# Optimization experiments

Hardware: AMD Instinct MI355X
Metric: run time of the kernel (lower is better)

The kernel has to match this reference:

```python
import jax, jax.numpy as jnp
import numpy as np

T, B, D, E, H = 64, 1024, 128, 256, 512


def _gru(x_emb, h0, W_ih, W_hh, b_ih, b_hh):
    """Standard GRU (PyTorch gate convention) over time-major x_emb [T,B,E]."""
    xW = x_emb @ W_ih + b_ih  # [T,B,3H], precompute input contractions

    def step(h, xw):
        hW = h @ W_hh + b_hh
        xr, xz, xn = jnp.split(xw, 3, axis=-1)
        hr, hz, hn = jnp.split(hW, 3, axis=-1)
        r = jax.nn.sigmoid(xr + hr)
        z = jax.nn.sigmoid(xz + hz)
        n = jnp.tanh(xn + r * hn)
        h_new = (1.0 - z) * n + z * h
        return h_new, h_new

    h_t, ys = jax.lax.scan(step, h0, xW)
    return ys, h_t


def setup_inputs() -> dict:
    key = jax.random.key(0)
    ks = jax.random.split(key, 16)
    s_in = 1.0 / np.sqrt(D)
    s_emb = 1.0 / np.sqrt(E)
    s_hid = 1.0 / np.sqrt(H)
    return {
        "past_input": jax.random.normal(ks[0], (T, B, D), jnp.float32),
        "future_input": jax.random.normal(ks[1], (T, B, D), jnp.float32),
        "noise": jax.random.normal(ks[2], (B, H), jnp.float32),
        "W_emb": jax.random.normal(ks[3], (D, E), jnp.float32) * s_in,
        "b_emb": jnp.zeros((E,), jnp.float32),
        "W_ih_enc": jax.random.normal(ks[4], (E, 3 * H), jnp.float32) * s_emb,
        "W_hh_enc": jax.random.normal(ks[5], (H, 3 * H), jnp.float32) * s_hid,
        "b_ih_enc": jnp.zeros((3 * H,), jnp.float32),
        "b_hh_enc": jnp.zeros((3 * H,), jnp.float32),
        "W_ih_dec": jax.random.normal(ks[6], (E, 3 * H), jnp.float32) * s_emb,
        "W_hh_dec": jax.random.normal(ks[7], (H, 3 * H), jnp.float32) * s_hid,
        "b_ih_dec": jnp.zeros((3 * H,), jnp.float32),
        "b_hh_dec": jnp.zeros((3 * H,), jnp.float32),
        "W_out": jax.random.normal(ks[8], (H, D), jnp.float32) * s_hid,
        "b_out": jnp.zeros((D,), jnp.float32),
    }


def reference(past_input, future_input, noise, W_emb, b_emb,
              W_ih_enc, W_hh_enc, b_ih_enc, b_hh_enc,
              W_ih_dec, W_hh_dec, b_ih_dec, b_hh_dec,
              W_out, b_out):
    past_emb = jax.nn.relu(past_input @ W_emb + b_emb)      # [T,B,E]
    fut_emb = jax.nn.relu(future_input @ W_emb + b_emb)     # [T,B,E]

    h0 = jnp.zeros((past_emb.shape[1], W_hh_enc.shape[0]), past_emb.dtype)
    _, h_t = _gru(past_emb, h0, W_ih_enc, W_hh_enc, b_ih_enc, b_hh_enc)

    # shift future embedding: step 0 -> zeros, step t -> emb at t-1
    fut_shift = jnp.concatenate([jnp.zeros_like(fut_emb[:1]), fut_emb[:-1]], axis=0)

    hidden = h_t + noise
    future_target, _ = _gru(fut_shift, hidden, W_ih_dec, W_hh_dec, b_ih_dec, b_hh_dec)
    return future_target @ W_out + b_out  # [T,B,D]
```

## Files before the change

kernel.cpp:

```cpp
#include <hip/hip_runtime.h>

typedef __bf16 bf16;
typedef __bf16 bf16x8 __attribute__((ext_vector_type(8)));
typedef float f32x4 __attribute__((ext_vector_type(4)));

#define Tt 64
#define Bb 1024
#define Dd 128
#define Ee 256
#define Hh 512
#define H3 1536

__device__ __forceinline__ float sigmf(float x) { return 1.0f / (1.0f + __expf(-x)); }
__device__ __forceinline__ float tanhfast(float x) {
    float e = __expf(2.0f * x);
    return 1.0f - 2.0f / (e + 1.0f);
}

#define LD_SC(dst, bp, OFF) \
    asm volatile("global_load_dwordx4 %0, %1, off offset:" #OFF " sc1" : "=v"(dst) : "v"(bp))
#define ST_SC(bp, OFF, val) \
    asm volatile("global_store_short %0, %1, off offset:" #OFF " sc1" :: "v"(bp), "v"(val))

__global__ void k_prep(const float* __restrict__ We, const float* __restrict__ Wie, const float* __restrict__ Whe,
                       const float* __restrict__ Wid, const float* __restrict__ Whd, const float* __restrict__ Wo,
                       bf16* __restrict__ dWe, bf16* __restrict__ dWie, bf16* __restrict__ dWhe,
                       bf16* __restrict__ dWid, bf16* __restrict__ dWhd, bf16* __restrict__ dWo) {
    long i = (long)blockIdx.x * 256 + threadIdx.x;
    const float* s;
    bf16* d;
    int K, N;
    if (i < 32768) { s = We; d = dWe; K = Dd; N = Ee; }
    else if ((i -= 32768) < 393216) { s = Wie; d = dWie; K = Ee; N = H3; }
    else if ((i -= 393216) < 786432) { s = Whe; d = dWhe; K = Hh; N = H3; }
    else if ((i -= 786432) < 393216) { s = Wid; d = dWid; K = Ee; N = H3; }
    else if ((i -= 393216) < 786432) { s = Whd; d = dWhd; K = Hh; N = H3; }
    else if ((i -= 786432) < 65536) { s = Wo; d = dWo; K = Hh; N = Dd; }
    else return;
    int n = (int)(i / K), k = (int)(i - (long)n * K);
    d[i] = (bf16)s[(size_t)k * N + n];
}

__global__ __launch_bounds__(256) void k_embed(const float* __restrict__ xP, const float* __restrict__ xF,
                                               const bf16* __restrict__ WT, const float* __restrict__ bias,
                                               bf16* __restrict__ oP, bf16* __restrict__ oF) {
    const int lane = threadIdx.x & 63, wv = threadIdx.x >> 6;
    const float* x = blockIdx.z ? xF : xP;
    bf16* o = blockIdx.z ? oF : oP;
    const int m0w = blockIdx.x * 128 + wv * 32;
    const int c0 = blockIdx.y * 64;
    const int koff = (lane >> 4) * 8;
    f32x4 acc[2][4];
#pragma unroll
    for (int m = 0; m < 2; ++m)
#pragma unroll
        for (int s = 0; s < 4; ++s) acc[m][s] = f32x4{0.f, 0.f, 0.f, 0.f};

    const float* xp0 = x + (size_t)(m0w + (lane & 15)) * Dd + koff;
#pragma unroll
    for (int kc = 0; kc < 4; ++kc) {
        bf16x8 a0, a1;
        {
            float4 f0 = *(const float4*)(xp0 + kc * 32);
            float4 f1 = *(const float4*)(xp0 + kc * 32 + 4);
            a0[0] = (bf16)f0.x; a0[1] = (bf16)f0.y; a0[2] = (bf16)f0.z; a0[3] = (bf16)f0.w;
            a0[4] = (bf16)f1.x; a0[5] = (bf16)f1.y; a0[6] = (bf16)f1.z; a0[7] = (bf16)f1.w;
            float4 g0 = *(const float4*)(xp0 + 16 * Dd + kc * 32);
            float4 g1 = *(const float4*)(xp0 + 16 * Dd + kc * 32 + 4);
            a1[0] = (bf16)g0.x; a1[1] = (bf16)g0.y; a1[2] = (bf16)g0.z; a1[3] = (bf16)g0.w;
            a1[4] = (bf16)g1.x; a1[5] = (bf16)g1.y; a1[6] = (bf16)g1.z; a1[7] = (bf16)g1.w;
        }
#pragma unroll
        for (int s = 0; s < 4; ++s) {
            bf16x8 b = *(const bf16x8*)(WT + (size_t)(c0 + s * 16 + (lane & 15)) * Dd + kc * 32 + koff);
            acc[0][s] = __builtin_amdgcn_mfma_f32_16x16x32_bf16(a0, b, acc[0][s], 0, 0, 0);
            acc[1][s] = __builtin_amdgcn_mfma_f32_16x16x32_bf16(a1, b, acc[1][s], 0, 0, 0);
        }
    }
#pragma unroll
    for (int m = 0; m < 2; ++m)
#pragma unroll
        for (int s = 0; s < 4; ++s) {
            int col = c0 + s * 16 + (lane & 15);
            float bv = bias[col];
#pragma unroll
            for (int r = 0; r < 4; ++r) {
                int row = m0w + m * 16 + (lane >> 4) * 4 + r;
                o[(size_t)row * Ee + col] = (bf16)fmaxf(acc[m][s][r] + bv, 0.0f);
            }
        }
}

__global__ __launch_bounds__(512, 1) void k_gru_all(
    const bf16* __restrict__ embP, const bf16* __restrict__ embF, const float* __restrict__ noise,
    const bf16* __restrict__ WihE, const bf16* __restrict__ WhhE,
    const float* __restrict__ bIhE, const float* __restrict__ bHhE,
    const bf16* __restrict__ WihD, const bf16* __restrict__ WhhD,
    const float* __restrict__ bIhD, const float* __restrict__ bHhD,
    bf16* __restrict__ hA, bf16* __restrict__ hB, bf16* __restrict__ ys, unsigned* __restrict__ flags) {
    __shared__ bf16 Wih[6 * 8 * 64 * 8];
    __shared__ bf16 Whh[6 * 16 * 64 * 8];
    const int tid = threadIdx.x;
    const int lane = tid & 63, wv = tid >> 6;
    const int bid = blockIdx.x;
    const int im = (bid & 7) * 2 + (bid >> 7);
    const int in = (bid >> 3) & 15;
    const int rh = wv >> 1, ch = wv & 1;
    const int rowb = im * 64 + rh * 16;
    const int arow0 = rowb + (lane & 15);
    const int koff = (lane >> 4) * 8;
    const int colc = in * 32 + ch * 16 + (lane & 15);
    unsigned* dom = flags + ((size_t)im * 4 + rh) * 32;
    const int myidx = in * 2 + ch;

    const bf16x8* WihV = (const bf16x8*)Wih;
    const bf16x8* WhhV = (const bf16x8*)Whh;

    auto stage = [&](const bf16* WT, int Kdim, int KC, bf16* lds) {
        int total = 6 * KC * 64;
        for (int idx = tid; idx < total; idx += 512) {
            int ln = idx & 63;
            int kc = (idx >> 6) % KC;
            int s = (idx >> 6) / KC;
            int gate = s >> 1, f = s & 1;
            int col = gate * Hh + in * 32 + f * 16 + (ln & 15);
            int k = kc * 32 + (ln >> 4) * 8;
            *(bf16x8*)(lds + (size_t)idx * 8) = *(const bf16x8*)(WT + (size_t)col * Kdim + k);
        }
    };

    float bi[3], bh[3];
    auto load_bias = [&](const float* bIh, const float* bHh) {
#pragma unroll
        for (int g = 0; g < 3; ++g) {
            bi[g] = bIh[g * Hh + colc];
            bh[g] = bHh[g * Hh + colc];
        }
    };

    auto signal = [&](unsigned seq) {
        asm volatile("s_waitcnt vmcnt(0)" ::: "memory");
        if (lane == 0) {
            unsigned* fp = dom + myidx;
            asm volatile("global_store_dword %0, %1, off sc1" :: "v"(fp), "v"(seq) : "memory");
        }
    };
    auto poll = [&](unsigned seq) -> unsigned long long {
        unsigned v;
        const unsigned* fp = dom + (lane & 31);
        asm volatile("global_load_dword %0, %1, off sc1\n\ts_waitcnt vmcnt(0)"
                     : "=v"(v) : "v"(fp) : "memory");
        return __ballot((int)(v >= seq));
    };
    auto wait_all = [&](unsigned seq) {
        while (poll(seq) != ~0ULL) __builtin_amdgcn_s_sleep(2);
    };

    f32x4 aR, aZ, aNX, aNH;
    auto zacc = [&]() {
        aR = f32x4{0.f, 0.f, 0.f, 0.f};
        aZ = f32x4{0.f, 0.f, 0.f, 0.f};
        aNX = f32x4{0.f, 0.f, 0.f, 0.f};
        aNH = f32x4{0.f, 0.f, 0.f, 0.f};
    };

    auto xp_phase = [&](const bf16* xp) {
        const bf16* ap = xp + (size_t)arow0 * Ee + koff;
#pragma unroll
        for (int kc = 0; kc < 8; ++kc) {
            bf16x8 a = *(const bf16x8*)(ap + kc * 32);
            aR = __builtin_amdgcn_mfma_f32_16x16x32_bf16(a, WihV[((0 + ch) * 8 + kc) * 64 + lane], aR, 0, 0, 0);
            aZ = __builtin_amdgcn_mfma_f32_16x16x32_bf16(a, WihV[((2 + ch) * 8 + kc) * 64 + lane], aZ, 0, 0, 0);
            aNX = __builtin_amdgcn_mfma_f32_16x16x32_bf16(a, WihV[((4 + ch) * 8 + kc) * 64 + lane], aNX, 0, 0, 0);
        }
    };

    auto hw_phase = [&](const bf16* hp, unsigned seq) {
        const bf16* h0p = hp + (size_t)arow0 * Hh + koff;
        bf16x8 h0[16];
        unsigned long long rdy = poll(seq);
#define HSTEP(p, OFF) \
        while (((rdy >> (2 * p)) & 3ULL) != 3ULL) { __builtin_amdgcn_s_sleep(2); rdy = poll(seq); } \
        LD_SC(h0[p], h0p, OFF);
        HSTEP(0, 0)    HSTEP(1, 64)   HSTEP(2, 128)  HSTEP(3, 192)
        HSTEP(4, 256)  HSTEP(5, 320)  HSTEP(6, 384)  HSTEP(7, 448)
        HSTEP(8, 512)  HSTEP(9, 576)  HSTEP(10, 640) HSTEP(11, 704)
        HSTEP(12, 768) HSTEP(13, 832) HSTEP(14, 896) HSTEP(15, 960)
#undef HSTEP
        asm volatile("s_waitcnt vmcnt(0)" ::: "memory");
        __builtin_amdgcn_sched_barrier(0);
#pragma unroll
        for (int kc = 0; kc < 16; ++kc) {
            aR = __builtin_amdgcn_mfma_f32_16x16x32_bf16(h0[kc], WhhV[((0 + ch) * 16 + kc) * 64 + lane], aR, 0, 0, 0);
            aZ = __builtin_amdgcn_mfma_f32_16x16x32_bf16(h0[kc], WhhV[((2 + ch) * 16 + kc) * 64 + lane], aZ, 0, 0, 0);
            aNH = __builtin_amdgcn_mfma_f32_16x16x32_bf16(h0[kc], WhhV[((4 + ch) * 16 + kc) * 64 + lane], aNH, 0, 0, 0);
        }
    };

    float hreg[4];
#pragma unroll
    for (int i = 0; i < 4; ++i) hreg[i] = 0.0f;

    auto epi = [&](bf16* op) {
        bf16* stb = op + (size_t)(rowb + (lane >> 4) * 4) * Hh + colc;
        unsigned short us[4];
#pragma unroll
        for (int r = 0; r < 4; ++r) {
            float rg = sigmf(aR[r] + bi[0] + bh[0]);
            float zg = sigmf(aZ[r] + bi[1] + bh[1]);
            float ng = tanhfast(aNX[r] + bi[2] + rg * (aNH[r] + bh[2]));
            float hv = (1.0f - zg) * ng + zg * hreg[r];
            hreg[r] = hv;
            us[r] = __builtin_bit_cast(unsigned short, (bf16)hv);
        }
        ST_SC(stb, 0, us[0]);
        ST_SC(stb, 1024, us[1]);
        ST_SC(stb, 2048, us[2]);
        ST_SC(stb, 3072, us[3]);
    };

    stage(WihE, Ee, 8, Wih);
    stage(WhhE, Hh, 16, Whh);
    load_bias(bIhE, bHhE);
    __syncthreads();

#pragma unroll 1
    for (int t = 0; t < Tt; ++t) {
        zacc();
        xp_phase(embP + (size_t)t * Bb * Ee);
        if (t > 0) hw_phase(((t - 1) & 1) ? hB : hA, (unsigned)t);
        epi((t & 1) ? hB : hA);
        signal((unsigned)(t + 1));
    }

    wait_all((unsigned)Tt);
    {
        bf16* stb = hA + (size_t)(rowb + (lane >> 4) * 4) * Hh + colc;
        unsigned short us[4];
#pragma unroll
        for (int r = 0; r < 4; ++r) {
            int row = rowb + (lane >> 4) * 4 + r;
            float v = hreg[r] + noise[(size_t)row * Hh + colc];
            hreg[r] = v;
            us[r] = __builtin_bit_cast(unsigned short, (bf16)v);
        }
        ST_SC(stb, 0, us[0]);
        ST_SC(stb, 1024, us[1]);
        ST_SC(stb, 2048, us[2]);
        ST_SC(stb, 3072, us[3]);
    }
    __syncthreads();
    stage(WihD, Ee, 8, Wih);
    stage(WhhD, Hh, 16, Whh);
    __syncthreads();
    load_bias(bIhD, bHhD);
    signal((unsigned)(Tt + 1));

#pragma unroll 1
    for (int t = 0; t < Tt; ++t) {
        zacc();
        if (t > 0) xp_phase(embF + (size_t)(t - 1) * Bb * Ee);
        hw_phase(t ? ys + (size_t)(t - 1) * Bb * Hh : hA, (unsigned)(Tt + 1 + t));
        epi(ys + (size_t)t * Bb * Hh);
        if (t < Tt - 1) signal((unsigned)(Tt + 2 + t));
    }
}

__global__ __launch_bounds__(256) void k_out(const bf16* __restrict__ ys, const bf16* __restrict__ WT,
                                             const float* __restrict__ bias, float* __restrict__ out) {
    const int lane = threadIdx.x & 63, wv = threadIdx.x >> 6;
    const int m0w = blockIdx.x * 256 + wv * 64;
    const int c0 = blockIdx.y * 64;
    const int koff = (lane >> 4) * 8;
    f32x4 acc[4][4];
#pragma unroll
    for (int m = 0; m < 4; ++m)
#pragma unroll
        for (int s = 0; s < 4; ++s) acc[m][s] = f32x4{0.f, 0.f, 0.f, 0.f};

    const bf16* ap = ys + (size_t)(m0w + (lane & 15)) * Hh + koff;
#pragma unroll
    for (int kc = 0; kc < 16; ++kc) {
        bf16x8 a0 = *(const bf16x8*)(ap + kc * 32);
        bf16x8 a1 = *(const bf16x8*)(ap + 16 * Hh + kc * 32);
        bf16x8 a2 = *(const bf16x8*)(ap + 32 * Hh + kc * 32);
        bf16x8 a3 = *(const bf16x8*)(ap + 48 * Hh + kc * 32);
#pragma unroll
        for (int s = 0; s < 4; ++s) {
            bf16x8 b = *(const bf16x8*)(WT + (size_t)(c0 + s * 16 + (lane & 15)) * Hh + kc * 32 + koff);
            acc[0][s] = __builtin_amdgcn_mfma_f32_16x16x32_bf16(a0, b, acc[0][s], 0, 0, 0);
            acc[1][s] = __builtin_amdgcn_mfma_f32_16x16x32_bf16(a1, b, acc[1][s], 0, 0, 0);
            acc[2][s] = __builtin_amdgcn_mfma_f32_16x16x32_bf16(a2, b, acc[2][s], 0, 0, 0);
            acc[3][s] = __builtin_amdgcn_mfma_f32_16x16x32_bf16(a3, b, acc[3][s], 0, 0, 0);
        }
    }
#pragma unroll
    for (int m = 0; m < 4; ++m)
#pragma unroll
        for (int s = 0; s < 4; ++s) {
            int col = c0 + s * 16 + (lane & 15);
            float bv = bias[col];
#pragma unroll
            for (int r = 0; r < 4; ++r) {
                int row = m0w + m * 16 + (lane >> 4) * 4 + r;
                out[(size_t)row * Dd + col] = acc[m][s][r] + bv;
            }
        }
}

extern "C" void kernel_launch(void* const* d_in, const int* in_sizes, int n_in,
                              void* d_out, int out_size, void* d_ws, size_t ws_size,
                              hipStream_t stream) {
    const float* past = (const float*)d_in[0];
    const float* fut = (const float*)d_in[1];
    const float* noise = (const float*)d_in[2];
    const float* W_emb = (const float*)d_in[3];
    const float* b_emb = (const float*)d_in[4];
    const float* W_ih_enc = (const float*)d_in[5];
    const float* W_hh_enc = (const float*)d_in[6];
    const float* b_ih_enc = (const float*)d_in[7];
    const float* b_hh_enc = (const float*)d_in[8];
    const float* W_ih_dec = (const float*)d_in[9];
    const float* W_hh_dec = (const float*)d_in[10];
    const float* b_ih_dec = (const float*)d_in[11];
    const float* b_hh_dec = (const float*)d_in[12];
    const float* W_out = (const float*)d_in[13];
    const float* b_out = (const float*)d_in[14];
    float* out = (float*)d_out;

    char* w = (char*)d_ws;
    auto alloc = [&](size_t bytes) {
        char* p = w;
        w += (bytes + 255) & ~(size_t)255;
        return p;
    };
    bf16* embP = (bf16*)alloc((size_t)Tt * Bb * Ee * 2);
    bf16* embF = (bf16*)alloc((size_t)Tt * Bb * Ee * 2);
    bf16* ys = (bf16*)alloc((size_t)Tt * Bb * Hh * 2);
    bf16* hA = (bf16*)alloc((size_t)Bb * Hh * 2);
    bf16* hB = (bf16*)alloc((size_t)Bb * Hh * 2);
    bf16* WembT = (bf16*)alloc((size_t)Ee * Dd * 2);
    bf16* WihEncT = (bf16*)alloc((size_t)H3 * Ee * 2);
    bf16* WhhEncT = (bf16*)alloc((size_t)H3 * Hh * 2);
    bf16* WihDecT = (bf16*)alloc((size_t)H3 * Ee * 2);
    bf16* WhhDecT = (bf16*)alloc((size_t)H3 * Hh * 2);
    bf16* WoutT = (bf16*)alloc((size_t)Dd * Hh * 2);
    unsigned* flags = (unsigned*)alloc(16 * 4 * 32 * sizeof(unsigned));

    k_prep<<<9600, 256, 0, stream>>>(W_emb, W_ih_enc, W_hh_enc, W_ih_dec, W_hh_dec, W_out,
                                     WembT, WihEncT, WhhEncT, WihDecT, WhhDecT, WoutT);

    k_embed<<<dim3(Tt * Bb / 128, Ee / 64, 2), 256, 0, stream>>>(past, fut, WembT, b_emb, embP, embF);

    hipMemsetAsync(flags, 0, 16 * 4 * 32 * sizeof(unsigned), stream);

    void* args[] = {(void*)&embP, (void*)&embF, (void*)&noise,
                    (void*)&WihEncT, (void*)&WhhEncT, (void*)&b_ih_enc, (void*)&b_hh_enc,
                    (void*)&WihDecT, (void*)&WhhDecT, (void*)&b_ih_dec, (void*)&b_hh_dec,
                    (void*)&hA, (void*)&hB, (void*)&ys, (void*)&flags};
    hipLaunchCooperativeKernel((const void*)k_gru_all, dim3(256), dim3(512), args, 0, stream);

    k_out<<<dim3(Tt * Bb / 256, Dd / 64), 256, 0, stream>>>(ys, WoutT, b_out, out);
}
```

Before: 1.040 ms.

## Restructure persistent GRU kernel: register-resident weights, LDS-staged hidden state, 32x32 MFMA

The recurrent kernel now keeps each wave's slice of the input and hidden weights in registers instead of LDS. Each block cooperatively stages its 32-row tile of the previous hidden state into swizzled LDS and runs 32x32x16 MFMAs. Gate pre-activations go through an LDS plane so four waves can run a vectorized epilogue that writes with dwordx4 stores. Synchronisation changes to one flag per block over 8 column-blocks instead of fine-grained per-wave polling. The aim is to cut LDS weight traffic and narrow store and poll overhead, at the cost of heavy register pressure (48 bf16x8 weight fragments per lane), extra block barriers and a coarser wait that can no longer overlap loads with partial readiness.

```diff
diff --git a/kernel.cpp b/kernel.cpp
--- a/kernel.cpp
+++ b/kernel.cpp
@@ -3,6 +3,7 @@
 typedef __bf16 bf16;
 typedef __bf16 bf16x8 __attribute__((ext_vector_type(8)));
 typedef float f32x4 __attribute__((ext_vector_type(4)));
+typedef float f32x16 __attribute__((ext_vector_type(16)));
 
 #define Tt 64
 #define Bb 1024
@@ -17,10 +18,10 @@
     return 1.0f - 2.0f / (e + 1.0f);
 }
 
-#define LD_SC(dst, bp, OFF) \
-    asm volatile("global_load_dwordx4 %0, %1, off offset:" #OFF " sc1" : "=v"(dst) : "v"(bp))
-#define ST_SC(bp, OFF, val) \
-    asm volatile("global_store_short %0, %1, off offset:" #OFF " sc1" :: "v"(bp), "v"(val))
+#define LD_SC(dst, bp) \
+    asm volatile("global_load_dwordx4 %0, %1, off sc1" : "=v"(dst) : "v"(bp))
+#define ST_SCX4(bp, val) \
+    asm volatile("global_store_dwordx4 %0, %1, off sc1" :: "v"(bp), "v"(val))
 
 __global__ void k_prep(const float* __restrict__ We, const float* __restrict__ Wie, const float* __restrict__ Whe,
                        const float* __restrict__ Wid, const float* __restrict__ Whd, const float* __restrict__ Wo,
@@ -91,177 +92,219 @@
         }
 }
 
-__global__ __launch_bounds__(512, 1) void k_gru_all(
+__global__ __launch_bounds__(384, 2) void k_gru_all(
     const bf16* __restrict__ embP, const bf16* __restrict__ embF, const float* __restrict__ noise,
     const bf16* __restrict__ WihE, const bf16* __restrict__ WhhE,
     const float* __restrict__ bIhE, const float* __restrict__ bHhE,
     const bf16* __restrict__ WihD, const bf16* __restrict__ WhhD,
     const float* __restrict__ bIhD, const float* __restrict__ bHhD,
     bf16* __restrict__ hA, bf16* __restrict__ hB, bf16* __restrict__ ys, unsigned* __restrict__ flags) {
-    __shared__ bf16 Wih[6 * 8 * 64 * 8];
-    __shared__ bf16 Whh[6 * 16 * 64 * 8];
+    __shared__ bf16 hS[32 * 512];
+    __shared__ float gS[4][32][68];
+    __shared__ float bT[64][4];
+
     const int tid = threadIdx.x;
     const int lane = tid & 63, wv = tid >> 6;
     const int bid = blockIdx.x;
-    const int im = (bid & 7) * 2 + (bid >> 7);
-    const int in = (bid >> 3) & 15;
-    const int rh = wv >> 1, ch = wv & 1;
-    const int rowb = im * 64 + rh * 16;
-    const int arow0 = rowb + (lane & 15);
-    const int koff = (lane >> 4) * 8;
-    const int colc = in * 32 + ch * 16 + (lane & 15);
-    unsigned* dom = flags + ((size_t)im * 4 + rh) * 32;
-    const int myidx = in * 2 + ch;
-
-    const bf16x8* WihV = (const bf16x8*)Wih;
-    const bf16x8* WhhV = (const bf16x8*)Whh;
-
-    auto stage = [&](const bf16* WT, int Kdim, int KC, bf16* lds) {
-        int total = 6 * KC * 64;
-        for (int idx = tid; idx < total; idx += 512) {
-            int ln = idx & 63;
-            int kc = (idx >> 6) % KC;
-            int s = (idx >> 6) / KC;
-            int gate = s >> 1, f = s & 1;
-            int col = gate * Hh + in * 32 + f * 16 + (ln & 15);
-            int k = kc * 32 + (ln >> 4) * 8;
-            *(bf16x8*)(lds + (size_t)idx * 8) = *(const bf16x8*)(WT + (size_t)col * Kdim + k);
-        }
-    };
-
-    float bi[3], bh[3];
-    auto load_bias = [&](const float* bIh, const float* bHh) {
-#pragma unroll
-        for (int g = 0; g < 3; ++g) {
-            bi[g] = bIh[g * Hh + colc];
-            bh[g] = bHh[g * Hh + colc];
+    const int im = bid & 31;
+    const int in = bid >> 5;
+    const int g = wv >> 1;
+    const int cn = wv & 1;
+    const int colT = in * 64 + cn * 32;
+    const int l31 = lane & 31, l5 = lane >> 5;
+    const int rowg0 = im * 32;
+    const unsigned rx = (unsigned)((l31 & 15) << 4);
+
+    unsigned* fbase = flags + (size_t)im * 8 * 16;
+
+    bf16x8 Bx[16], Bh[32];
+    auto load_B = [&](const bf16* WihT, const bf16* WhhT) {
+        const bf16* px = WihT + (size_t)(g * Hh + colT + l31) * Ee + l5 * 8;
+#pragma unroll
+        for (int kf = 0; kf < 16; ++kf) Bx[kf] = *(const bf16x8*)(px + kf * 16);
+        const bf16* ph = WhhT + (size_t)(g * Hh + colT + l31) * Hh + l5 * 8;
+#pragma unroll
+        for (int kf = 0; kf < 32; ++kf) Bh[kf] = *(const bf16x8*)(ph + kf * 16);
+    };
+
+    auto build_bias = [&](const float* bIh, const float* bHh) {
+        for (int c = tid; c < 64; c += 384) {
+            int col = in * 64 + c;
+            bT[c][0] = bIh[col] + bHh[col];
+            bT[c][1] = bIh[Hh + col] + bHh[Hh + col];
+            bT[c][2] = bIh[2 * Hh + col];
+            bT[c][3] = bHh[2 * Hh + col];
         }
     };
 
     auto signal = [&](unsigned seq) {
         asm volatile("s_waitcnt vmcnt(0)" ::: "memory");
-        if (lane == 0) {
-            unsigned* fp = dom + myidx;
+        __syncthreads();
+        if (tid == 0) {
+            unsigned* fp = fbase + in * 16;
             asm volatile("global_store_dword %0, %1, off sc1" :: "v"(fp), "v"(seq) : "memory");
         }
     };
-    auto poll = [&](unsigned seq) -> unsigned long long {
-        unsigned v;
-        const unsigned* fp = dom + (lane & 31);
-        asm volatile("global_load_dword %0, %1, off sc1\n\ts_waitcnt vmcnt(0)"
-                     : "=v"(v) : "v"(fp) : "memory");
-        return __ballot((int)(v >= seq));
-    };
     auto wait_all = [&](unsigned seq) {
-        while (poll(seq) != ~0ULL) __builtin_amdgcn_s_sleep(2);
-    };
-
-    f32x4 aR, aZ, aNX, aNH;
+        const unsigned* fp = fbase + (lane & 7) * 16;
+        for (;;) {
+            unsigned v;
+            asm volatile("global_load_dword %0, %1, off sc1\n\ts_waitcnt vmcnt(0)"
+                         : "=v"(v) : "v"(fp) : "memory");
+            if (__all((int)(v >= seq))) break;
+            __builtin_amdgcn_s_sleep(2);
+        }
+    };
+
+    auto stage = [&](const bf16* hp, unsigned seq) {
+        wait_all(seq);
+        bf16x8 v[6];
+#pragma unroll
+        for (int u0 = 0; u0 < 3; ++u0) {
+            int u = wv + u0 * 6;
+            if (u < 16) {
+                int p = u >> 1, hh = u & 1;
+#pragma unroll
+                for (int i = 0; i < 2; ++i) {
+                    int idx = i * 64 + lane;
+                    int r = hh * 16 + (idx >> 3), cg = idx & 7;
+                    const bf16* ga = hp + (size_t)(rowg0 + r) * Hh + p * 64 + cg * 8;
+                    LD_SC(v[u0 * 2 + i], ga);
+                }
+            }
+        }
+        asm volatile("s_waitcnt vmcnt(0)" ::: "memory");
+#pragma unroll
+        for (int u0 = 0; u0 < 3; ++u0) {
+            int u = wv + u0 * 6;
+            if (u < 16) {
+                int p = u >> 1, hh = u & 1;
+#pragma unroll
+                for (int i = 0; i < 2; ++i) {
+                    int idx = i * 64 + lane;
+                    int r = hh * 16 + (idx >> 3), cg = idx & 7;
+                    unsigned byte = ((unsigned)r << 10) + ((((unsigned)p << 7) + ((unsigned)cg << 4)) ^ ((unsigned)(r & 15) << 4));
+                    *(bf16x8*)((char*)hS + byte) = v[u0 * 2 + i];
+                }
+            }
+        }
+    };
+
+    f32x16 C0, C1;
     auto zacc = [&]() {
-        aR = f32x4{0.f, 0.f, 0.f, 0.f};
-        aZ = f32x4{0.f, 0.f, 0.f, 0.f};
-        aNX = f32x4{0.f, 0.f, 0.f, 0.f};
-        aNH = f32x4{0.f, 0.f, 0.f, 0.f};
-    };
-
+#pragma unroll
+        for (int i = 0; i < 16; ++i) { C0[i] = 0.f; C1[i] = 0.f; }
+    };
     auto xp_phase = [&](const bf16* xp) {
-        const bf16* ap = xp + (size_t)arow0 * Ee + koff;
-#pragma unroll
-        for (int kc = 0; kc < 8; ++kc) {
-            bf16x8 a = *(const bf16x8*)(ap + kc * 32);
-            aR = __builtin_amdgcn_mfma_f32_16x16x32_bf16(a, WihV[((0 + ch) * 8 + kc) * 64 + lane], aR, 0, 0, 0);
-            aZ = __builtin_amdgcn_mfma_f32_16x16x32_bf16(a, WihV[((2 + ch) * 8 + kc) * 64 + lane], aZ, 0, 0, 0);
-            aNX = __builtin_amdgcn_mfma_f32_16x16x32_bf16(a, WihV[((4 + ch) * 8 + kc) * 64 + lane], aNX, 0, 0, 0);
-        }
-    };
-
-    auto hw_phase = [&](const bf16* hp, unsigned seq) {
-        const bf16* h0p = hp + (size_t)arow0 * Hh + koff;
-        bf16x8 h0[16];
-        unsigned long long rdy = poll(seq);
-#define HSTEP(p, OFF) \
-        while (((rdy >> (2 * p)) & 3ULL) != 3ULL) { __builtin_amdgcn_s_sleep(2); rdy = poll(seq); } \
-        LD_SC(h0[p], h0p, OFF);
-        HSTEP(0, 0)    HSTEP(1, 64)   HSTEP(2, 128)  HSTEP(3, 192)
-        HSTEP(4, 256)  HSTEP(5, 320)  HSTEP(6, 384)  HSTEP(7, 448)
-        HSTEP(8, 512)  HSTEP(9, 576)  HSTEP(10, 640) HSTEP(11, 704)
-        HSTEP(12, 768) HSTEP(13, 832) HSTEP(14, 896) HSTEP(15, 960)
-#undef HSTEP
-        asm volatile("s_waitcnt vmcnt(0)" ::: "memory");
-        __builtin_amdgcn_sched_barrier(0);
-#pragma unroll
-        for (int kc = 0; kc < 16; ++kc) {
-            aR = __builtin_amdgcn_mfma_f32_16x16x32_bf16(h0[kc], WhhV[((0 + ch) * 16 + kc) * 64 + lane], aR, 0, 0, 0);
-            aZ = __builtin_amdgcn_mfma_f32_16x16x32_bf16(h0[kc], WhhV[((2 + ch) * 16 + kc) * 64 + lane], aZ, 0, 0, 0);
-            aNH = __builtin_amdgcn_mfma_f32_16x16x32_bf16(h0[kc], WhhV[((4 + ch) * 16 + kc) * 64 + lane], aNH, 0, 0, 0);
-        }
-    };
-
-    float hreg[4];
-#pragma unroll
-    for (int i = 0; i < 4; ++i) hreg[i] = 0.0f;
+        const bf16* ap = xp + (size_t)(rowg0 + l31) * Ee + l5 * 8;
+#pragma unroll
+        for (int kf = 0; kf < 16; ++kf) {
+            bf16x8 a = *(const bf16x8*)(ap + kf * 16);
+            C0 = __builtin_amdgcn_mfma_f32_32x32x16_bf16(a, Bx[kf], C0, 0, 0, 0);
+        }
+    };
+    auto hw_phase = [&]() {
+        const unsigned rb = (unsigned)(l31 << 10);
+        if (g == 2) {
+#pragma unroll
+            for (int kf = 0; kf < 32; ++kf) {
+                unsigned off = rb + (((unsigned)(kf * 32 + (l5 << 4))) ^ rx);
+                bf16x8 a = *(const bf16x8*)((const char*)hS + off);
+                C1 = __builtin_amdgcn_mfma_f32_32x32x16_bf16(a, Bh[kf], C1, 0, 0, 0);
+            }
+        } else {
+#pragma unroll
+            for (int kf = 0; kf < 32; ++kf) {
+                unsigned off = rb + (((unsigned)(kf * 32 + (l5 << 4))) ^ rx);
+                bf16x8 a = *(const bf16x8*)((const char*)hS + off);
+                C0 = __builtin_amdgcn_mfma_f32_32x32x16_bf16(a, Bh[kf], C0, 0, 0, 0);
+            }
+        }
+    };
+    auto plane_write = [&]() {
+#pragma unroll
+        for (int i = 0; i < 16; ++i) {
+            int row = (i & 3) + 8 * (i >> 2) + 4 * l5;
+            gS[g][row][cn * 32 + l31] = C0[i];
+            if (g == 2) gS[3][row][cn * 32 + l31] = C1[i];
+        }
+    };
+
+    float hreg[8];
+#pragma unroll
+    for (int i = 0; i < 8; ++i) hreg[i] = 0.0f;
+    const int erow = wv * 8 + (lane >> 3);
+    const int cb = (lane & 7) * 8;
 
     auto epi = [&](bf16* op) {
-        bf16* stb = op + (size_t)(rowb + (lane >> 4) * 4) * Hh + colc;
-        unsigned short us[4];
-#pragma unroll
-        for (int r = 0; r < 4; ++r) {
-            float rg = sigmf(aR[r] + bi[0] + bh[0]);
-            float zg = sigmf(aZ[r] + bi[1] + bh[1]);
-            float ng = tanhfast(aNX[r] + bi[2] + rg * (aNH[r] + bh[2]));
-            float hv = (1.0f - zg) * ng + zg * hreg[r];
-            hreg[r] = hv;
-            us[r] = __builtin_bit_cast(unsigned short, (bf16)hv);
-        }
-        ST_SC(stb, 0, us[0]);
-        ST_SC(stb, 1024, us[1]);
-        ST_SC(stb, 2048, us[2]);
-        ST_SC(stb, 3072, us[3]);
-    };
-
-    stage(WihE, Ee, 8, Wih);
-    stage(WhhE, Hh, 16, Whh);
-    load_bias(bIhE, bHhE);
-    __syncthreads();
+        float4 R0 = *(const float4*)&gS[0][erow][cb], R1 = *(const float4*)&gS[0][erow][cb + 4];
+        float4 Z0 = *(const float4*)&gS[1][erow][cb], Z1 = *(const float4*)&gS[1][erow][cb + 4];
+        float4 X0 = *(const float4*)&gS[2][erow][cb], X1 = *(const float4*)&gS[2][erow][cb + 4];
+        float4 H0 = *(const float4*)&gS[3][erow][cb], H1 = *(const float4*)&gS[3][erow][cb + 4];
+        bf16x8 o;
+#pragma unroll
+        for (int j = 0; j < 8; ++j) {
+            float pr = (j < 4) ? R0[j & 3] : R1[j & 3];
+            float pz = (j < 4) ? Z0[j & 3] : Z1[j & 3];
+            float px = (j < 4) ? X0[j & 3] : X1[j & 3];
+            float ph = (j < 4) ? H0[j & 3] : H1[j & 3];
+            float4 bt = *(const float4*)&bT[cb + j][0];
+            float rg = sigmf(pr + bt.x);
+            float zg = sigmf(pz + bt.y);
+            float ng = tanhfast(px + bt.z + rg * (ph + bt.w));
+            float hv = (1.0f - zg) * ng + zg * hreg[j];
+            hreg[j] = hv;
+            o[j] = (bf16)hv;
+        }
+        bf16* sp = op + (size_t)(rowg0 + erow) * Hh + in * 64 + cb;
+        ST_SCX4(sp, o);
+    };
+
+    load_B(WihE, WhhE);
+    build_bias(bIhE, bHhE);
 
 #pragma unroll 1
     for (int t = 0; t < Tt; ++t) {
+        if (t > 0) stage((t & 1) ? hB : hA, (unsigned)t);
+        __syncthreads();
         zacc();
         xp_phase(embP + (size_t)t * Bb * Ee);
-        if (t > 0) hw_phase(((t - 1) & 1) ? hB : hA, (unsigned)t);
-        epi((t & 1) ? hB : hA);
+        if (t > 0) hw_phase();
+        plane_write();
+        __syncthreads();
+        if (wv < 4) epi(((t + 1) & 1) ? hB : hA);
         signal((unsigned)(t + 1));
     }
 
     wait_all((unsigned)Tt);
-    {
-        bf16* stb = hA + (size_t)(rowb + (lane >> 4) * 4) * Hh + colc;
-        unsigned short us[4];
-#pragma unroll
-        for (int r = 0; r < 4; ++r) {
-            int row = rowb + (lane >> 4) * 4 + r;
-            float v = hreg[r] + noise[(size_t)row * Hh + colc];
-            hreg[r] = v;
-            us[r] = __builtin_bit_cast(unsigned short, (bf16)v);
-        }
-        ST_SC(stb, 0, us[0]);
-        ST_SC(stb, 1024, us[1]);
-        ST_SC(stb, 2048, us[2]);
-        ST_SC(stb, 3072, us[3]);
+    if (wv < 4) {
+        const float* np = noise + (size_t)(rowg0 + erow) * Hh + in * 64 + cb;
+        float4 n0 = *(const float4*)np;
+        float4 n1 = *(const float4*)(np + 4);
+        bf16x8 o;
+#pragma unroll
+        for (int j = 0; j < 8; ++j) {
+            float v = hreg[j] + ((j < 4) ? n0[j & 3] : n1[j & 3]);
+            hreg[j] = v;
+            o[j] = (bf16)v;
+        }
+        bf16* sp = hB + (size_t)(rowg0 + erow) * Hh + in * 64 + cb;
+        ST_SCX4(sp, o);
     }
-    __syncthreads();
-    stage(WihD, Ee, 8, Wih);
-    stage(WhhD, Hh, 16, Whh);
-    __syncthreads();
-    load_bias(bIhD, bHhD);
+    load_B(WihD, WhhD);
+    build_bias(bIhD, bHhD);
     signal((unsigned)(Tt + 1));
 
 #pragma unroll 1
     for (int t = 0; t < Tt; ++t) {
+        stage(t ? ys + (size_t)(t - 1) * Bb * Hh : hB, (unsigned)(Tt + 1 + t));
+        __syncthreads();
         zacc();
         if (t > 0) xp_phase(embF + (size_t)(t - 1) * Bb * Ee);
-        hw_phase(t ? ys + (size_t)(t - 1) * Bb * Hh : hA, (unsigned)(Tt + 1 + t));
-        epi(ys + (size_t)t * Bb * Hh);
+        hw_phase();
+        plane_write();
+        __syncthreads();
+        if (wv < 4) epi(ys + (size_t)t * Bb * Hh);
         if (t < Tt - 1) signal((unsigned)(Tt + 2 + t));
     }
 }
@@ -345,20 +388,20 @@
     bf16* WihDecT = (bf16*)alloc((size_t)H3 * Ee * 2);
     bf16* WhhDecT = (bf16*)alloc((size_t)H3 * Hh * 2);
     bf16* WoutT = (bf16*)alloc((size_t)Dd * Hh * 2);
-    unsigned* flags = (unsigned*)alloc(16 * 4 * 32 * sizeof(unsigned));
+    unsigned* flags = (unsigned*)alloc(32 * 8 * 16 * sizeof(unsigned));
 
     k_prep<<<9600, 256, 0, stream>>>(W_emb, W_ih_enc, W_hh_enc, W_ih_dec, W_hh_dec, W_out,
                                      WembT, WihEncT, WhhEncT, WihDecT, WhhDecT, WoutT);
 
     k_embed<<<dim3(Tt * Bb / 128, Ee / 64, 2), 256, 0, stream>>>(past, fut, WembT, b_emb, embP, embF);
 
-    hipMemsetAsync(flags, 0, 16 * 4 * 32 * sizeof(unsigned), stream);
+    hipMemsetAsync(flags, 0, 32 * 8 * 16 * sizeof(unsigned), stream);
 
     void* args[] = {(void*)&embP, (void*)&embF, (void*)&noise,
                     (void*)&WihEncT, (void*)&WhhEncT, (void*)&b_ih_enc, (void*)&b_hh_enc,
                     (void*)&WihDecT, (void*)&WhhDecT, (void*)&b_ih_dec, (void*)&b_hh_dec,
                     (void*)&hA, (void*)&hB, (void*)&ys, (void*)&flags};
-    hipLaunchCooperativeKernel((const void*)k_gru_all, dim3(256), dim3(512), args, 0, stream);
+    hipLaunchCooperativeKernel((const void*)k_gru_all, dim3(256), dim3(384), args, 0, stream);
 
     k_out<<<dim3(Tt * Bb / 256, Dd / 64), 256, 0, stream>>>(ys, WoutT, b_out, out);
 }
```

Measured after the change: 2.927 ms. 2.81x slower.

## Merge column-half waves so each wave computes both 16-column halves of GRU tile

Applied to the files above, without the earlier changes.

The persistent GRU kernel drops from 8 to 4 waves per block. Each wave now computes both 16-column halves of its 32-column slice, sharing one A-fragment load (input and h) across twice the MFMAs. This halves the number of waves that poll flags and load h from global memory, and the flag layout is padded to one flag per 64-byte slot to cut false sharing. The cost is less wave-level parallelism per CU and more accumulator registers per wave, which may expose MFMA and epilogue latency on the serial recurrence path.

```diff
diff --git a/kernel.cpp b/kernel.cpp
--- a/kernel.cpp
+++ b/kernel.cpp
@@ -18,7 +18,7 @@
 }
 
 #define LD_SC(dst, bp, OFF) \
-    asm volatile("global_load_dwordx4 %0, %1, off offset:" #OFF " sc1" : "=v"(dst) : "v"(bp))
+    asm volatile("global_load_dwordx4 %0, %1, off offset:" #OFF " sc1" : "=&v"(dst) : "v"(bp))
 #define ST_SC(bp, OFF, val) \
     asm volatile("global_store_short %0, %1, off offset:" #OFF " sc1" :: "v"(bp), "v"(val))
 
@@ -91,7 +91,7 @@
         }
 }
 
-__global__ __launch_bounds__(512, 1) void k_gru_all(
+__global__ __launch_bounds__(256, 1) void k_gru_all(
     const bf16* __restrict__ embP, const bf16* __restrict__ embF, const float* __restrict__ noise,
     const bf16* __restrict__ WihE, const bf16* __restrict__ WhhE,
     const float* __restrict__ bIhE, const float* __restrict__ bHhE,
@@ -101,24 +101,22 @@
     __shared__ bf16 Wih[6 * 8 * 64 * 8];
     __shared__ bf16 Whh[6 * 16 * 64 * 8];
     const int tid = threadIdx.x;
-    const int lane = tid & 63, wv = tid >> 6;
+    const int lane = tid & 63, rh = tid >> 6;
     const int bid = blockIdx.x;
     const int im = (bid & 7) * 2 + (bid >> 7);
     const int in = (bid >> 3) & 15;
-    const int rh = wv >> 1, ch = wv & 1;
     const int rowb = im * 64 + rh * 16;
     const int arow0 = rowb + (lane & 15);
     const int koff = (lane >> 4) * 8;
-    const int colc = in * 32 + ch * 16 + (lane & 15);
-    unsigned* dom = flags + ((size_t)im * 4 + rh) * 32;
-    const int myidx = in * 2 + ch;
+    const int colc0 = in * 32 + (lane & 15);
+    unsigned* dom = flags + ((size_t)im * 4 + rh) * 16 * 16;
 
     const bf16x8* WihV = (const bf16x8*)Wih;
     const bf16x8* WhhV = (const bf16x8*)Whh;
 
     auto stage = [&](const bf16* WT, int Kdim, int KC, bf16* lds) {
         int total = 6 * KC * 64;
-        for (int idx = tid; idx < total; idx += 512) {
+        for (int idx = tid; idx < total; idx += 256) {
             int ln = idx & 63;
             int kc = (idx >> 6) % KC;
             int s = (idx >> 6) / KC;
@@ -129,39 +127,45 @@
         }
     };
 
-    float bi[3], bh[3];
+    float bi[3][2], bh[3][2];
     auto load_bias = [&](const float* bIh, const float* bHh) {
 #pragma unroll
-        for (int g = 0; g < 3; ++g) {
-            bi[g] = bIh[g * Hh + colc];
-            bh[g] = bHh[g * Hh + colc];
-        }
+        for (int g = 0; g < 3; ++g)
+#pragma unroll
+            for (int f = 0; f < 2; ++f) {
+                int c = g * Hh + colc0 + f * 16;
+                bi[g][f] = bIh[c];
+                bh[g][f] = bHh[c];
+            }
     };
 
     auto signal = [&](unsigned seq) {
         asm volatile("s_waitcnt vmcnt(0)" ::: "memory");
         if (lane == 0) {
-            unsigned* fp = dom + myidx;
+            unsigned* fp = dom + in * 16;
             asm volatile("global_store_dword %0, %1, off sc1" :: "v"(fp), "v"(seq) : "memory");
         }
     };
     auto poll = [&](unsigned seq) -> unsigned long long {
         unsigned v;
-        const unsigned* fp = dom + (lane & 31);
+        const unsigned* fp = dom + (lane & 15) * 16;
         asm volatile("global_load_dword %0, %1, off sc1\n\ts_waitcnt vmcnt(0)"
-                     : "=v"(v) : "v"(fp) : "memory");
+                     : "=&v"(v) : "v"(fp) : "memory");
         return __ballot((int)(v >= seq));
     };
     auto wait_all = [&](unsigned seq) {
         while (poll(seq) != ~0ULL) __builtin_amdgcn_s_sleep(2);
     };
 
-    f32x4 aR, aZ, aNX, aNH;
+    f32x4 aR[2], aZ[2], aNX[2], aNH[2];
     auto zacc = [&]() {
-        aR = f32x4{0.f, 0.f, 0.f, 0.f};
-        aZ = f32x4{0.f, 0.f, 0.f, 0.f};
-        aNX = f32x4{0.f, 0.f, 0.f, 0.f};
-        aNH = f32x4{0.f, 0.f, 0.f, 0.f};
+#pragma unroll
+        for (int f = 0; f < 2; ++f) {
+            aR[f] = f32x4{0.f, 0.f, 0.f, 0.f};
+            aZ[f] = f32x4{0.f, 0.f, 0.f, 0.f};
+            aNX[f] = f32x4{0.f, 0.f, 0.f, 0.f};
+            aNH[f] = f32x4{0.f, 0.f, 0.f, 0.f};
+        }
     };
 
     auto xp_phase = [&](const bf16* xp) {
@@ -169,9 +173,12 @@
 #pragma unroll
         for (int kc = 0; kc < 8; ++kc) {
             bf16x8 a = *(const bf16x8*)(ap + kc * 32);
-            aR = __builtin_amdgcn_mfma_f32_16x16x32_bf16(a, WihV[((0 + ch) * 8 + kc) * 64 + lane], aR, 0, 0, 0);
-            aZ = __builtin_amdgcn_mfma_f32_16x16x32_bf16(a, WihV[((2 + ch) * 8 + kc) * 64 + lane], aZ, 0, 0, 0);
-            aNX = __builtin_amdgcn_mfma_f32_16x16x32_bf16(a, WihV[((4 + ch) * 8 + kc) * 64 + lane], aNX, 0, 0, 0);
+#pragma unroll
+            for (int f = 0; f < 2; ++f) {
+                aR[f] = __builtin_amdgcn_mfma_f32_16x16x32_bf16(a, WihV[((0 + f) * 8 + kc) * 64 + lane], aR[f], 0, 0, 0);
+                aZ[f] = __builtin_amdgcn_mfma_f32_16x16x32_bf16(a, WihV[((2 + f) * 8 + kc) * 64 + lane], aZ[f], 0, 0, 0);
+                aNX[f] = __builtin_amdgcn_mfma_f32_16x16x32_bf16(a, WihV[((4 + f) * 8 + kc) * 64 + lane], aNX[f], 0, 0, 0);
+            }
         }
     };
 
@@ -180,7 +187,7 @@
         bf16x8 h0[16];
         unsigned long long rdy = poll(seq);
 #define HSTEP(p, OFF) \
-        while (((rdy >> (2 * p)) & 3ULL) != 3ULL) { __builtin_amdgcn_s_sleep(2); rdy = poll(seq); } \
+        while (!((rdy >> p) & 1ULL)) { __builtin_amdgcn_s_sleep(2); rdy = poll(seq); } \
         LD_SC(h0[p], h0p, OFF);
         HSTEP(0, 0)    HSTEP(1, 64)   HSTEP(2, 128)  HSTEP(3, 192)
         HSTEP(4, 256)  HSTEP(5, 320)  HSTEP(6, 384)  HSTEP(7, 448)
@@ -191,32 +198,38 @@
         __builtin_amdgcn_sched_barrier(0);
 #pragma unroll
         for (int kc = 0; kc < 16; ++kc) {
-            aR = __builtin_amdgcn_mfma_f32_16x16x32_bf16(h0[kc], WhhV[((0 + ch) * 16 + kc) * 64 + lane], aR, 0, 0, 0);
-            aZ = __builtin_amdgcn_mfma_f32_16x16x32_bf16(h0[kc], WhhV[((2 + ch) * 16 + kc) * 64 + lane], aZ, 0, 0, 0);
-            aNH = __builtin_amdgcn_mfma_f32_16x16x32_bf16(h0[kc], WhhV[((4 + ch) * 16 + kc) * 64 + lane], aNH, 0, 0, 0);
-        }
-    };
-
-    float hreg[4];
-#pragma unroll
-    for (int i = 0; i < 4; ++i) hreg[i] = 0.0f;
+#pragma unroll
+            for (int f = 0; f < 2; ++f) {
+                aR[f] = __builtin_amdgcn_mfma_f32_16x16x32_bf16(h0[kc], WhhV[((0 + f) * 16 + kc) * 64 + lane], aR[f], 0, 0, 0);
+                aZ[f] = __builtin_amdgcn_mfma_f32_16x16x32_bf16(h0[kc], WhhV[((2 + f) * 16 + kc) * 64 + lane], aZ[f], 0, 0, 0);
+                aNH[f] = __builtin_amdgcn_mfma_f32_16x16x32_bf16(h0[kc], WhhV[((4 + f) * 16 + kc) * 64 + lane], aNH[f], 0, 0, 0);
+            }
+        }
+    };
+
+    float hreg[8];
+#pragma unroll
+    for (int i = 0; i < 8; ++i) hreg[i] = 0.0f;
 
     auto epi = [&](bf16* op) {
-        bf16* stb = op + (size_t)(rowb + (lane >> 4) * 4) * Hh + colc;
-        unsigned short us[4];
-#pragma unroll
-        for (int r = 0; r < 4; ++r) {
-            float rg = sigmf(aR[r] + bi[0] + bh[0]);
-            float zg = sigmf(aZ[r] + bi[1] + bh[1]);
-            float ng = tanhfast(aNX[r] + bi[2] + rg * (aNH[r] + bh[2]));
-            float hv = (1.0f - zg) * ng + zg * hreg[r];
-            hreg[r] = hv;
-            us[r] = __builtin_bit_cast(unsigned short, (bf16)hv);
-        }
-        ST_SC(stb, 0, us[0]);
-        ST_SC(stb, 1024, us[1]);
-        ST_SC(stb, 2048, us[2]);
-        ST_SC(stb, 3072, us[3]);
+#pragma unroll
+        for (int f = 0; f < 2; ++f) {
+            bf16* stb = op + (size_t)(rowb + (lane >> 4) * 4) * Hh + colc0 + f * 16;
+            unsigned short us[4];
+#pragma unroll
+            for (int r = 0; r < 4; ++r) {
+                float rg = sigmf(aR[f][r] + bi[0][f] + bh[0][f]);
+                float zg = sigmf(aZ[f][r] + bi[1][f] + bh[1][f]);
+                float ng = tanhfast(aNX[f][r] + bi[2][f] + rg * (aNH[f][r] + bh[2][f]));
+                float hv = (1.0f - zg) * ng + zg * hreg[f * 4 + r];
+                hreg[f * 4 + r] = hv;
+                us[r] = __builtin_bit_cast(unsigned short, (bf16)hv);
+            }
+            ST_SC(stb, 0, us[0]);
+            ST_SC(stb, 1024, us[1]);
+            ST_SC(stb, 2048, us[2]);
+            ST_SC(stb, 3072, us[3]);
+        }
     };
 
     stage(WihE, Ee, 8, Wih);
@@ -235,19 +248,22 @@
 
     wait_all((unsigned)Tt);
     {
-        bf16* stb = hA + (size_t)(rowb + (lane >> 4) * 4) * Hh + colc;
-        unsigned short us[4];
-#pragma unroll
-        for (int r = 0; r < 4; ++r) {
-            int row = rowb + (lane >> 4) * 4 + r;
-            float v = hreg[r] + noise[(size_t)row * Hh + colc];
-            hreg[r] = v;
-            us[r] = __builtin_bit_cast(unsigned short, (bf16)v);
-        }
-        ST_SC(stb, 0, us[0]);
-        ST_SC(stb, 1024, us[1]);
-        ST_SC(stb, 2048, us[2]);
-        ST_SC(stb, 3072, us[3]);
+#pragma unroll
+        for (int f = 0; f < 2; ++f) {
+            bf16* stb = hA + (size_t)(rowb + (lane >> 4) * 4) * Hh + colc0 + f * 16;
+            unsigned short us[4];
+#pragma unroll
+            for (int r = 0; r < 4; ++r) {
+                int row = rowb + (lane >> 4) * 4 + r;
+                float v = hreg[f * 4 + r] + noise[(size_t)row * Hh + colc0 + f * 16];
+                hreg[f * 4 + r] = v;
+                us[r] = __builtin_bit_cast(unsigned short, (bf16)v);
+            }
+            ST_SC(stb, 0, us[0]);
+            ST_SC(stb, 1024, us[1]);
+            ST_SC(stb, 2048, us[2]);
+            ST_SC(stb, 3072, us[3]);
+        }
     }
     __syncthreads();
     stage(WihD, Ee, 8, Wih);
@@ -345,20 +361,20 @@
     bf16* WihDecT = (bf16*)alloc((size_t)H3 * Ee * 2);
     bf16* WhhDecT = (bf16*)alloc((size_t)H3 * Hh * 2);
     bf16* WoutT = (bf16*)alloc((size_t)Dd * Hh * 2);
-    unsigned* flags = (unsigned*)alloc(16 * 4 * 32 * sizeof(unsigned));
+    unsigned* flags = (unsigned*)alloc(16 * 4 * 16 * 16 * sizeof(unsigned));
 
     k_prep<<<9600, 256, 0, stream>>>(W_emb, W_ih_enc, W_hh_enc, W_ih_dec, W_hh_dec, W_out,
                                      WembT, WihEncT, WhhEncT, WihDecT, WhhDecT, WoutT);
 
     k_embed<<<dim3(Tt * Bb / 128, Ee / 64, 2), 256, 0, stream>>>(past, fut, WembT, b_emb, embP, embF);
 
-    hipMemsetAsync(flags, 0, 16 * 4 * 32 * sizeof(unsigned), stream);
+    hipMemsetAsync(flags, 0, 16 * 4 * 16 * 16 * sizeof(unsigned), stream);
 
     void* args[] = {(void*)&embP, (void*)&embF, (void*)&noise,
                     (void*)&WihEncT, (void*)&WhhEncT, (void*)&b_ih_enc, (void*)&b_hh_enc,
                     (void*)&WihDecT, (void*)&WhhDecT, (void*)&b_ih_dec, (void*)&b_hh_dec,
                     (void*)&hA, (void*)&hB, (void*)&ys, (void*)&flags};
-    hipLaunchCooperativeKernel((const void*)k_gru_all, dim3(256), dim3(512), args, 0, stream);
+    hipLaunchCooperativeKernel((const void*)k_gru_all, dim3(256), dim3(256), args, 0, stream);
 
     k_out<<<dim3(Tt * Bb / 256, Dd / 64), 256, 0, stream>>>(ys, WoutT, b_out, out);
 }
```

New measurement: 1.004 ms, median of 3. 1.04x faster.
